# Kernel optimization log

Measured on AMD Instinct MI355X. Metric: run time of the kernel, lower is better.

Reference implementation:

```python
import jax, jax.numpy as jnp
import numpy as np

HID = 768
POS = 768
TGT = 20
LBL = 30522
EPS = 1e-5


def layer_norm(x, g, b):
    mu = jnp.mean(x, axis=-1, keepdims=True)
    var = jnp.mean((x - mu) ** 2, axis=-1, keepdims=True)
    return (x - mu) * jax.lax.rsqrt(var + EPS) * g + b


def setup_inputs() -> dict:
    key = jax.random.key(0)
    ks = jax.random.split(key, 12)
    bs, n_node, num_pairs = 4, 512, 128
    inp = {
        "input_nodes": jax.random.normal(ks[0], (bs, n_node, HID), dtype=jnp.float32),
        "pairs": jax.random.randint(ks[1], (bs, num_pairs, 2), 0, n_node - 1, dtype=jnp.int64),
        "pos_emb": jax.random.normal(ks[2], (TGT, POS), dtype=jnp.float32) * 0.02,
        "W1": jax.random.normal(ks[3], (2 * HID + POS, HID), dtype=jnp.float32) * 0.02,
        "b1": jnp.zeros((HID,), dtype=jnp.float32),
        "g1": jnp.ones((HID,), dtype=jnp.float32),
        "be1": jnp.zeros((HID,), dtype=jnp.float32),
        "W2": jax.random.normal(ks[4], (HID, HID), dtype=jnp.float32) * 0.02,
        "b2": jnp.zeros((HID,), dtype=jnp.float32),
        "g2": jnp.ones((HID,), dtype=jnp.float32),
        "be2": jnp.zeros((HID,), dtype=jnp.float32),
        "Wd": jax.random.normal(ks[5], (HID, LBL), dtype=jnp.float32) * 0.02,
        "bd": jnp.zeros((LBL,), dtype=jnp.float32),
    }
    return inp


def reference(input_nodes, pairs, pos_emb, W1, b1, g1, be1, W2, b2, g2, be2, Wd, bd):
    bs, num_pairs, _ = pairs.shape
    dim = input_nodes.shape[-1]
    left = pairs[:, :, 0] + 1   # [bs, np]
    right = pairs[:, :, 1] + 1
    # gather paired node features: [bs, np, dim]
    lh = jnp.take_along_axis(input_nodes, left[:, :, None], axis=1)
    rh = jnp.take_along_axis(input_nodes, right[:, :, None], axis=1)
    R = bs * num_pairs
    lh = jnp.broadcast_to(lh.reshape(R, 1, dim), (R, TGT, dim))
    rh = jnp.broadcast_to(rh.reshape(R, 1, dim), (R, TGT, dim))
    pe = jnp.broadcast_to(pos_emb[None, :, :], (R, TGT, POS))
    x = jnp.concatenate((lh, rh, pe), axis=-1)  # [R, TGT, 2*HID+POS]
    h = layer_norm(jax.nn.gelu(x @ W1 + b1), g1, be1)
    h = layer_norm(jax.nn.gelu(h @ W2 + b2), g2, be2)
    return h @ Wd + bd  # [R, TGT, LBL]
```

## Files before the change

kernel.cpp:

```cpp
#include <hip/hip_runtime.h>
#include <stdint.h>
#include <math.h>

typedef unsigned short u16;
typedef unsigned int u32;

#define HID   768
#define TGT   20
#define LBL   30522
#define RPAIR 512
#define ROWS  10240
#define KCAT  1536
#define NPAD  30592

typedef float  f32x4  __attribute__((ext_vector_type(4)));
typedef __bf16 bf16x8 __attribute__((ext_vector_type(8)));

__device__ __forceinline__ u16 f2bf(float f) {
  u32 u = __float_as_uint(f);
  u += 0x7fffu + ((u >> 16) & 1u);
  return (u16)(u >> 16);
}
__device__ __forceinline__ float bf2f(u16 h) {
  return __uint_as_float(((u32)h) << 16);
}
__device__ __forceinline__ float gelu_tanh(float x) {
  float x3 = x * x * x;
  float t = tanhf(0.7978845608028654f * (x + 0.044715f * x3));
  return 0.5f * x * (1.0f + t);
}

__device__ __forceinline__ void async16(u16* lds, const u16* g) {
  __builtin_amdgcn_global_load_lds(
      (__attribute__((address_space(1))) void*)const_cast<u16*>(g),
      (__attribute__((address_space(3))) void*)lds,
      16, 0, 0);
}

__global__ __launch_bounds__(256) void tconv_kernel(const float* __restrict__ B,
                                                    u16* __restrict__ Bt,
                                                    int K, int N, int Npad) {
  __shared__ u16 tile[32][34];
  int n0 = blockIdx.x * 32, k0 = blockIdx.y * 32;
  int tx = threadIdx.x & 31, ty = threadIdx.x >> 5;
#pragma unroll
  for (int i = 0; i < 4; i++) {
    int kk = ty + i * 8;
    int k = k0 + kk, n = n0 + tx;
    float v = (k < K && n < N) ? B[(size_t)k * N + n] : 0.0f;
    tile[kk][tx] = f2bf(v);
  }
  __syncthreads();
#pragma unroll
  for (int i = 0; i < 4; i++) {
    int nn = ty + i * 8;
    int n = n0 + nn, k = k0 + tx;
    if (n < Npad && k < K) Bt[(size_t)n * K + k] = tile[tx][nn];
  }
}

__global__ __launch_bounds__(256) void gather_kernel(const float* __restrict__ nodes,
                                                     const int* __restrict__ p32,
                                                     u16* __restrict__ A1) {
  int idx = blockIdx.x * 256 + threadIdx.x;
  if (idx >= RPAIR * KCAT) return;
  bool is64 = ((p32[1] | p32[3] | p32[5] | p32[7] | p32[9] | p32[11] | p32[13] | p32[15]) == 0);
  int r = idx / KCAT, c = idx - r * KCAT;
  int b = r >> 7, p = r & 127;
  int which = (c >= HID) ? 1 : 0;
  int cc = which ? (c - HID) : c;
  int slot = (b * 128 + p) * 2 + which;
  int node = (is64 ? p32[slot * 2] : p32[slot]) + 1;
  float v = nodes[((size_t)(b * 512 + node)) * HID + cc];
  A1[idx] = f2bf(v);
}

__global__ __launch_bounds__(256) void peproj_kernel(const float* __restrict__ pos_emb,
                                                     const float* __restrict__ W1,
                                                     const float* __restrict__ b1,
                                                     float* __restrict__ pep) {
  __shared__ float pe[HID];
  int t = blockIdx.x, tid = threadIdx.x;
  for (int i = tid; i < HID; i += 256) pe[i] = pos_emb[t * HID + i];
  __syncthreads();
  float acc0 = 0.f, acc1 = 0.f, acc2 = 0.f;
  const float* Wp = W1 + (size_t)KCAT * HID;
  for (int k = 0; k < HID; k++) {
    float p = pe[k];
    const float* wr = Wp + (size_t)k * HID;
    acc0 = fmaf(p, wr[tid], acc0);
    acc1 = fmaf(p, wr[tid + 256], acc1);
    acc2 = fmaf(p, wr[tid + 512], acc2);
  }
  pep[t * HID + tid]       = acc0 + b1[tid];
  pep[t * HID + tid + 256] = acc1 + b1[tid + 256];
  pep[t * HID + tid + 512] = acc2 + b1[tid + 512];
}

template <int EPI>
__global__ __launch_bounds__(256) void gemm_bt(const u16* __restrict__ A,
                                               const u16* __restrict__ Bt,
                                               const float* __restrict__ bias,
                                               float* __restrict__ Cf,
                                               u16* __restrict__ Cb,
                                               int N, int K) {
  __shared__ __align__(16) u16 As[128 * 32];
  __shared__ __align__(16) u16 Bs[128 * 32];
  const int tid  = threadIdx.x;
  const int lane = tid & 63;
  const int w    = tid >> 6;
  const int wr   = w >> 1, wc = w & 1;
  const int m0 = blockIdx.y * 128;
  const int n0 = blockIdx.x * 128;

  f32x4 acc[4][4];
  const f32x4 fzero = {0.f, 0.f, 0.f, 0.f};
#pragma unroll
  for (int m = 0; m < 4; m++)
#pragma unroll
    for (int n = 0; n < 4; n++) acc[m][n] = fzero;

  const int srow = lane >> 2;
  const int scol = (lane & 3) * 8;
  const int nkt = K >> 5;

  for (int kt = 0; kt < nkt; ++kt) {
    const int k0 = kt << 5;
#pragma unroll
    for (int j = 0; j < 2; j++) {
      int rbase = w * 32 + j * 16;
      async16(&As[rbase * 32], A + (size_t)(m0 + rbase + srow) * K + k0 + scol);
      async16(&Bs[rbase * 32], Bt + (size_t)(n0 + rbase + srow) * K + k0 + scol);
    }
    asm volatile("s_waitcnt vmcnt(0)" ::: "memory");
    __syncthreads();

    bf16x8 a[4], b[4];
    const int kk = (lane >> 4) * 8;
#pragma unroll
    for (int m = 0; m < 4; m++)
      a[m] = *reinterpret_cast<const bf16x8*>(&As[(wr * 64 + m * 16 + (lane & 15)) * 32 + kk]);
#pragma unroll
    for (int n = 0; n < 4; n++)
      b[n] = *reinterpret_cast<const bf16x8*>(&Bs[(wc * 64 + n * 16 + (lane & 15)) * 32 + kk]);
#pragma unroll
    for (int m = 0; m < 4; m++)
#pragma unroll
      for (int n = 0; n < 4; n++)
        acc[m][n] = __builtin_amdgcn_mfma_f32_16x16x32_bf16(a[m], b[n], acc[m][n], 0, 0, 0);
    __syncthreads();
  }

  const int rr = (lane >> 4) * 4;
  const int cc = lane & 15;
#pragma unroll
  for (int m = 0; m < 4; m++) {
#pragma unroll
    for (int n = 0; n < 4; n++) {
      int col = n0 + wc * 64 + n * 16 + cc;
#pragma unroll
      for (int j = 0; j < 4; j++) {
        int row = m0 + wr * 64 + m * 16 + rr + j;
        float v = acc[m][n][j];
        if (EPI == 0) {
          Cf[(size_t)row * N + col] = v;
        } else if (EPI == 1) {
          v = gelu_tanh(v + bias[col]);
          Cb[(size_t)row * N + col] = f2bf(v);
        } else {
          if (col < N) Cf[(size_t)row * N + col] = v + bias[col];
        }
      }
    }
  }
}

__global__ __launch_bounds__(256) void fuse1_kernel(const float* __restrict__ s,
                                                    const float* __restrict__ pep,
                                                    const float* __restrict__ g1,
                                                    const float* __restrict__ be1,
                                                    u16* __restrict__ h1) {
  __shared__ float red[8];
  int g = blockIdx.x, tid = threadIdx.x;
  int r = g / TGT, t = g - r * TGT;
  const float* sr = s + (size_t)r * HID;
  const float* pt = pep + (size_t)t * HID;
  float y[3], s1 = 0.f, s2 = 0.f;
#pragma unroll
  for (int i = 0; i < 3; i++) {
    int j = tid + i * 256;
    float x = sr[j] + pt[j];
    y[i] = gelu_tanh(x);
    s1 += y[i];
    s2 += y[i] * y[i];
  }
#pragma unroll
  for (int off = 32; off > 0; off >>= 1) {
    s1 += __shfl_down(s1, off);
    s2 += __shfl_down(s2, off);
  }
  if ((tid & 63) == 0) { red[tid >> 6] = s1; red[4 + (tid >> 6)] = s2; }
  __syncthreads();
  float mean = (red[0] + red[1] + red[2] + red[3]) * (1.0f / HID);
  float var  = (red[4] + red[5] + red[6] + red[7]) * (1.0f / HID) - mean * mean;
  float inv  = rsqrtf(var + 1e-5f);
#pragma unroll
  for (int i = 0; i < 3; i++) {
    int j = tid + i * 256;
    h1[(size_t)g * HID + j] = f2bf((y[i] - mean) * inv * g1[j] + be1[j]);
  }
}

__global__ __launch_bounds__(256) void fuse2_kernel(const u16* __restrict__ G,
                                                    const float* __restrict__ g2,
                                                    const float* __restrict__ be2,
                                                    u16* __restrict__ h2) {
  __shared__ float red[8];
  int g = blockIdx.x, tid = threadIdx.x;
  const u16* gr = G + (size_t)g * HID;
  float y[3], s1 = 0.f, s2 = 0.f;
#pragma unroll
  for (int i = 0; i < 3; i++) {
    int j = tid + i * 256;
    y[i] = bf2f(gr[j]);
    s1 += y[i];
    s2 += y[i] * y[i];
  }
#pragma unroll
  for (int off = 32; off > 0; off >>= 1) {
    s1 += __shfl_down(s1, off);
    s2 += __shfl_down(s2, off);
  }
  if ((tid & 63) == 0) { red[tid >> 6] = s1; red[4 + (tid >> 6)] = s2; }
  __syncthreads();
  float mean = (red[0] + red[1] + red[2] + red[3]) * (1.0f / HID);
  float var  = (red[4] + red[5] + red[6] + red[7]) * (1.0f / HID) - mean * mean;
  float inv  = rsqrtf(var + 1e-5f);
#pragma unroll
  for (int i = 0; i < 3; i++) {
    int j = tid + i * 256;
    h2[(size_t)g * HID + j] = f2bf((y[i] - mean) * inv * g2[j] + be2[j]);
  }
}

extern "C" void kernel_launch(void* const* d_in, const int* in_sizes, int n_in,
                              void* d_out, int out_size, void* d_ws, size_t ws_size,
                              hipStream_t stream) {
  const float* input_nodes = (const float*)d_in[0];
  const int*   pairs       = (const int*)d_in[1];
  const float* pos_emb     = (const float*)d_in[2];
  const float* W1  = (const float*)d_in[3];
  const float* b1  = (const float*)d_in[4];
  const float* g1  = (const float*)d_in[5];
  const float* be1 = (const float*)d_in[6];
  const float* W2  = (const float*)d_in[7];
  const float* b2  = (const float*)d_in[8];
  const float* g2  = (const float*)d_in[9];
  const float* be2 = (const float*)d_in[10];
  const float* Wd  = (const float*)d_in[11];
  const float* bd  = (const float*)d_in[12];
  float* out = (float*)d_out;

  char* ws = (char*)d_ws;
  u16*   WdT   = (u16*)(ws + 0);
  u16*   W2T   = (u16*)(ws + 46989312);
  u16*   W1lrT = (u16*)(ws + 48168960);
  u16*   A1    = (u16*)(ws + 50528256);
  float* pep   = (float*)(ws + 52101120);
  float* sbuf  = (float*)(ws + 52162560);
  u16*   h1    = (u16*)(ws + 53735424);
  u16*   G     = (u16*)(ws + 69464064);
  u16*   h2    = (u16*)(ws + 85192704);

  tconv_kernel<<<dim3(956, 24), 256, 0, stream>>>(Wd, WdT, HID, LBL, NPAD);
  tconv_kernel<<<dim3(24, 24), 256, 0, stream>>>(W2, W2T, HID, HID, HID);
  tconv_kernel<<<dim3(24, 48), 256, 0, stream>>>(W1, W1lrT, KCAT, HID, HID);
  gather_kernel<<<dim3((RPAIR * KCAT + 255) / 256), 256, 0, stream>>>(input_nodes, pairs, A1);
  peproj_kernel<<<dim3(TGT), 256, 0, stream>>>(pos_emb, W1, b1, pep);

  gemm_bt<0><<<dim3(6, 4), 256, 0, stream>>>(A1, W1lrT, nullptr, sbuf, nullptr, HID, KCAT);
  fuse1_kernel<<<dim3(ROWS), 256, 0, stream>>>(sbuf, pep, g1, be1, h1);

  gemm_bt<1><<<dim3(6, 80), 256, 0, stream>>>(h1, W2T, b2, nullptr, G, HID, HID);
  fuse2_kernel<<<dim3(ROWS), 256, 0, stream>>>(G, g2, be2, h2);

  gemm_bt<2><<<dim3(239, 80), 256, 0, stream>>>(h2, WdT, bd, out, nullptr, LBL, HID);
}
```

Before: 1.070 ms.

## Replace head GEMM with 256x256-tile double-buffered MFMA kernel

Adds a dedicated 512-thread kernel for the large vocabulary projection. It uses 256x256 output tiles, XOR-swizzled LDS, async global-to-LDS loads, split-phase double buffering with raised MFMA priority, and an XCD-aware block remap. Wd is padded to 30720 columns so tiles divide evenly, and fuse2 now writes its output in place into G, dropping the h2 buffer. The aim is more operand reuse and better overlap of loads with MFMA in the dominant GEMM. The cost is higher register and LDS pressure, and more fragile hand scheduling with explicit waitcnt.

```diff
diff --git a/kernel.cpp b/kernel.cpp
--- a/kernel.cpp
+++ b/kernel.cpp
@@ -11,7 +11,7 @@
 #define RPAIR 512
 #define ROWS  10240
 #define KCAT  1536
-#define NPAD  30592
+#define NPAD2 30720
 
 typedef float  f32x4  __attribute__((ext_vector_type(4)));
 typedef __bf16 bf16x8 __attribute__((ext_vector_type(8)));
@@ -36,6 +36,8 @@
       (__attribute__((address_space(3))) void*)lds,
       16, 0, 0);
 }
+
+#define BARRIER() do { asm volatile("" ::: "memory"); __builtin_amdgcn_s_barrier(); asm volatile("" ::: "memory"); } while (0)
 
 __global__ __launch_bounds__(256) void tconv_kernel(const float* __restrict__ B,
                                                     u16* __restrict__ Bt,
@@ -164,13 +166,159 @@
         float v = acc[m][n][j];
         if (EPI == 0) {
           Cf[(size_t)row * N + col] = v;
-        } else if (EPI == 1) {
+        } else {
           v = gelu_tanh(v + bias[col]);
           Cb[(size_t)row * N + col] = f2bf(v);
-        } else {
-          if (col < N) Cf[(size_t)row * N + col] = v + bias[col];
         }
       }
+    }
+  }
+}
+
+__global__ __launch_bounds__(512, 2) void gemm256_head(const u16* __restrict__ A,
+                                                       const u16* __restrict__ B,
+                                                       const float* __restrict__ bias,
+                                                       float* __restrict__ C) {
+  __shared__ __align__(16) u16 As[2][256 * 64];
+  __shared__ __align__(16) u16 Bs[2][256 * 64];
+  const int tid  = threadIdx.x;
+  const int lane = tid & 63;
+  const int wid  = tid >> 6;
+  const int wm   = wid >> 2;
+  const int wn   = wid & 3;
+
+  int orig = blockIdx.x;
+  int l = (orig & 7) * 600 + (orig >> 3);
+  int mt = l / 120, nt = l - mt * 120;
+  const int m0 = mt * 256, n0 = nt * 256;
+  const int nkt = 12;
+
+  f32x4 acc[8][4];
+  const f32x4 fzero = {0.f, 0.f, 0.f, 0.f};
+#pragma unroll
+  for (int mi = 0; mi < 8; mi++)
+#pragma unroll
+    for (int ni = 0; ni < 4; ni++) acc[mi][ni] = fzero;
+
+  const int sl_r = lane >> 3;
+  const int sl_c = ((lane & 7) ^ sl_r) * 8;
+  auto stage_half = [&](const u16* src, int grow0, u16* ldsReg, int half, int ke0) {
+#pragma unroll
+    for (int j = 0; j < 2; j++) {
+      int rowb = half * 128 + (j * 8 + wid) * 8;
+      const u16* gp = src + (size_t)(grow0 + rowb + sl_r) * 768 + ke0 + sl_c;
+      async16(ldsReg + rowb * 64, gp);
+    }
+  };
+  auto lda = [&](const u16* buf, int mi, int ks) -> bf16x8 {
+    int row = wm * 128 + mi * 16 + (lane & 15);
+    int kch = ks * 4 + (lane >> 4);
+    return *reinterpret_cast<const bf16x8*>(&buf[row * 64 + ((kch ^ (row & 7)) << 3)]);
+  };
+  auto ldb = [&](const u16* buf, int ni, int ks) -> bf16x8 {
+    int row = wn * 64 + ni * 16 + (lane & 15);
+    int kch = ks * 4 + (lane >> 4);
+    return *reinterpret_cast<const bf16x8*>(&buf[row * 64 + ((kch ^ (row & 7)) << 3)]);
+  };
+
+  stage_half(A, m0, As[0], 0, 0);
+  stage_half(A, m0, As[0], 1, 0);
+  stage_half(B, n0, Bs[0], 0, 0);
+  stage_half(B, n0, Bs[0], 1, 0);
+  stage_half(A, m0, As[1], 0, 64);
+  stage_half(A, m0, As[1], 1, 64);
+  asm volatile("s_waitcnt vmcnt(4)" ::: "memory");
+  __builtin_amdgcn_sched_barrier(0);
+  __builtin_amdgcn_s_barrier();
+  asm volatile("" ::: "memory");
+
+  bf16x8 aF[8][2];
+  bf16x8 bF[4][2];
+
+#define MFMA_QUAD(MI0, NI0)                                                        \
+  do {                                                                             \
+    __builtin_amdgcn_s_setprio(1);                                                 \
+    _Pragma("unroll") for (int mi = (MI0); mi < (MI0) + 4; ++mi)                   \
+      _Pragma("unroll") for (int ni = (NI0); ni < (NI0) + 2; ++ni)                 \
+        _Pragma("unroll") for (int ks = 0; ks < 2; ++ks)                           \
+          acc[mi][ni] = __builtin_amdgcn_mfma_f32_16x16x32_bf16(aF[mi][ks], bF[ni][ks], acc[mi][ni], 0, 0, 0); \
+    __builtin_amdgcn_s_setprio(0);                                                 \
+  } while (0)
+
+#define WAIT_LGKM() do { asm volatile("s_waitcnt lgkmcnt(0)" ::: "memory"); __builtin_amdgcn_sched_barrier(0); } while (0)
+
+  for (int t = 0; t < nkt; ++t) {
+    const u16* Ab = As[t & 1];
+    const u16* Bb = Bs[t & 1];
+    u16* Bnext = Bs[(t + 1) & 1];
+    u16* Acur  = As[t & 1];
+    const int ke1 = (t + 1) * 64, ke2 = (t + 2) * 64;
+    const bool sB = (t + 1) < nkt, sA = (t + 2) < nkt;
+
+#pragma unroll
+    for (int mi = 0; mi < 4; ++mi)
+#pragma unroll
+      for (int ks = 0; ks < 2; ++ks) aF[mi][ks] = lda(Ab, mi, ks);
+#pragma unroll
+    for (int ni = 0; ni < 2; ++ni)
+#pragma unroll
+      for (int ks = 0; ks < 2; ++ks) bF[ni][ks] = ldb(Bb, ni, ks);
+    if (sB) stage_half(B, n0, Bnext, 0, ke1);
+    BARRIER();
+    WAIT_LGKM();
+    MFMA_QUAD(0, 0);
+    BARRIER();
+
+#pragma unroll
+    for (int mi = 4; mi < 8; ++mi)
+#pragma unroll
+      for (int ks = 0; ks < 2; ++ks) aF[mi][ks] = lda(Ab, mi, ks);
+    if (sB) stage_half(B, n0, Bnext, 1, ke1);
+    BARRIER();
+    WAIT_LGKM();
+    MFMA_QUAD(4, 0);
+    BARRIER();
+
+#pragma unroll
+    for (int ni = 2; ni < 4; ++ni)
+#pragma unroll
+      for (int ks = 0; ks < 2; ++ks) bF[ni][ks] = ldb(Bb, ni, ks);
+    if (sA) stage_half(A, m0, Acur, 0, ke2);
+    BARRIER();
+    WAIT_LGKM();
+    MFMA_QUAD(4, 2);
+    BARRIER();
+
+    if (sA) stage_half(A, m0, Acur, 1, ke2);
+    BARRIER();
+    MFMA_QUAD(0, 2);
+    if (t + 2 < nkt) {
+      asm volatile("s_waitcnt vmcnt(4)" ::: "memory");
+    } else if (t + 1 < nkt) {
+      asm volatile("s_waitcnt vmcnt(0)" ::: "memory");
+    }
+    __builtin_amdgcn_sched_barrier(0);
+    BARRIER();
+  }
+#undef MFMA_QUAD
+#undef WAIT_LGKM
+
+  const int r0 = m0 + wm * 128;
+  const int c0 = n0 + wn * 64;
+  const int rr = (lane >> 4) * 4;
+  const int ccl = lane & 15;
+#pragma unroll
+  for (int ni = 0; ni < 4; ++ni) {
+    int col = c0 + ni * 16 + ccl;
+    if (col < LBL) {
+      float bv = bias[col];
+#pragma unroll
+      for (int mi = 0; mi < 8; ++mi)
+#pragma unroll
+        for (int j = 0; j < 4; ++j) {
+          int row = r0 + mi * 16 + rr + j;
+          C[(size_t)row * LBL + col] = acc[mi][ni][j] + bv;
+        }
     }
   }
 }
@@ -263,16 +411,15 @@
 
   char* ws = (char*)d_ws;
   u16*   WdT   = (u16*)(ws + 0);
-  u16*   W2T   = (u16*)(ws + 46989312);
-  u16*   W1lrT = (u16*)(ws + 48168960);
-  u16*   A1    = (u16*)(ws + 50528256);
-  float* pep   = (float*)(ws + 52101120);
-  float* sbuf  = (float*)(ws + 52162560);
-  u16*   h1    = (u16*)(ws + 53735424);
-  u16*   G     = (u16*)(ws + 69464064);
-  u16*   h2    = (u16*)(ws + 85192704);
-
-  tconv_kernel<<<dim3(956, 24), 256, 0, stream>>>(Wd, WdT, HID, LBL, NPAD);
+  u16*   W2T   = (u16*)(ws + 47185920);
+  u16*   W1lrT = (u16*)(ws + 48365568);
+  u16*   A1    = (u16*)(ws + 50724864);
+  float* pep   = (float*)(ws + 52297728);
+  float* sbuf  = (float*)(ws + 52359168);
+  u16*   h1    = (u16*)(ws + 53932032);
+  u16*   G     = (u16*)(ws + 69660672);
+
+  tconv_kernel<<<dim3(960, 24), 256, 0, stream>>>(Wd, WdT, HID, LBL, NPAD2);
   tconv_kernel<<<dim3(24, 24), 256, 0, stream>>>(W2, W2T, HID, HID, HID);
   tconv_kernel<<<dim3(24, 48), 256, 0, stream>>>(W1, W1lrT, KCAT, HID, HID);
   gather_kernel<<<dim3((RPAIR * KCAT + 255) / 256), 256, 0, stream>>>(input_nodes, pairs, A1);
@@ -282,7 +429,7 @@
   fuse1_kernel<<<dim3(ROWS), 256, 0, stream>>>(sbuf, pep, g1, be1, h1);
 
   gemm_bt<1><<<dim3(6, 80), 256, 0, stream>>>(h1, W2T, b2, nullptr, G, HID, HID);
-  fuse2_kernel<<<dim3(ROWS), 256, 0, stream>>>(G, g2, be2, h2);
-
-  gemm_bt<2><<<dim3(239, 80), 256, 0, stream>>>(h2, WdT, bd, out, nullptr, LBL, HID);
-}
+  fuse2_kernel<<<dim3(ROWS), 256, 0, stream>>>(G, g2, be2, G);
+
+  gemm256_head<<<dim3(4800), 512, 0, stream>>>(G, WdT, bd, out);
+}
```

Result: slower. 1.296 ms (+21.1%).

## Add dedicated double-buffered head GEMM with XCD-aware tile mapping

Applied to the files above, without the earlier changes.

Replaces the generic gemm_bt<2> used for the large vocabulary projection with a specialized kernel. The new kernel double-buffers LDS with async copies so the next K-tile loads while the current one computes, and hardcodes K=768. It remaps a 1D block id so that each XCD handles a contiguous band of M tiles, which should improve L2 reuse of A. It also hoists the bias load per column and writes fuse2's output in place over G, dropping the separate h2 buffer. In exchange it doubles LDS use per block, which may lower occupancy.

```diff
diff --git a/kernel.cpp b/kernel.cpp
--- a/kernel.cpp
+++ b/kernel.cpp
@@ -164,13 +164,102 @@
         float v = acc[m][n][j];
         if (EPI == 0) {
           Cf[(size_t)row * N + col] = v;
-        } else if (EPI == 1) {
+        } else {
           v = gelu_tanh(v + bias[col]);
           Cb[(size_t)row * N + col] = f2bf(v);
-        } else {
-          if (col < N) Cf[(size_t)row * N + col] = v + bias[col];
         }
       }
+    }
+  }
+}
+
+__global__ __launch_bounds__(256) void gemm128_head(const u16* __restrict__ A,
+                                                    const u16* __restrict__ B,
+                                                    const float* __restrict__ bias,
+                                                    float* __restrict__ C) {
+  __shared__ __align__(16) u16 As[2][128 * 64];
+  __shared__ __align__(16) u16 Bs[2][128 * 64];
+  const int tid  = threadIdx.x;
+  const int lane = tid & 63;
+  const int w    = tid >> 6;
+  const int wr   = w >> 1, wc = w & 1;
+
+  const int bid   = blockIdx.x;
+  const int xcd   = bid & 7;
+  const int idx   = bid >> 3;
+  const int ntile = idx / 10;
+  const int mtile = xcd * 10 + (idx - ntile * 10);
+  const int m0 = mtile * 128;
+  const int n0 = ntile * 128;
+
+  f32x4 acc[4][4];
+  const f32x4 fzero = {0.f, 0.f, 0.f, 0.f};
+#pragma unroll
+  for (int m = 0; m < 4; m++)
+#pragma unroll
+    for (int n = 0; n < 4; n++) acc[m][n] = fzero;
+
+  const int sl_r = lane >> 3;
+  const int sl_c = ((lane & 7) ^ sl_r) * 8;
+  auto stage = [&](int buf, int kt) {
+    const int k0 = kt * 64;
+#pragma unroll
+    for (int j = 0; j < 4; j++) {
+      int rbase = w * 32 + j * 8;
+      async16(&As[buf][rbase * 64], A + (size_t)(m0 + rbase + sl_r) * 768 + k0 + sl_c);
+      async16(&Bs[buf][rbase * 64], B + (size_t)(n0 + rbase + sl_r) * 768 + k0 + sl_c);
+    }
+  };
+  auto lda = [&](const u16* buf, int m, int ks) -> bf16x8 {
+    int row = wr * 64 + m * 16 + (lane & 15);
+    int kch = ks * 4 + (lane >> 4);
+    return *reinterpret_cast<const bf16x8*>(&buf[row * 64 + ((kch ^ (row & 7)) << 3)]);
+  };
+  auto ldb = [&](const u16* buf, int n, int ks) -> bf16x8 {
+    int row = wc * 64 + n * 16 + (lane & 15);
+    int kch = ks * 4 + (lane >> 4);
+    return *reinterpret_cast<const bf16x8*>(&buf[row * 64 + ((kch ^ (row & 7)) << 3)]);
+  };
+
+  const int nkt = 12;
+  stage(0, 0);
+  __syncthreads();
+
+  for (int t = 0; t < nkt; ++t) {
+    const int cur = t & 1;
+    if (t + 1 < nkt) stage(cur ^ 1, t + 1);
+    const u16* Ab = As[cur];
+    const u16* Bb = Bs[cur];
+#pragma unroll
+    for (int ks = 0; ks < 2; ++ks) {
+      bf16x8 a[4], b[4];
+#pragma unroll
+      for (int m = 0; m < 4; m++) a[m] = lda(Ab, m, ks);
+#pragma unroll
+      for (int n = 0; n < 4; n++) b[n] = ldb(Bb, n, ks);
+#pragma unroll
+      for (int m = 0; m < 4; m++)
+#pragma unroll
+        for (int n = 0; n < 4; n++)
+          acc[m][n] = __builtin_amdgcn_mfma_f32_16x16x32_bf16(a[m], b[n], acc[m][n], 0, 0, 0);
+    }
+    __syncthreads();
+  }
+
+  const int rr = (lane >> 4) * 4;
+  const int cc = lane & 15;
+#pragma unroll
+  for (int n = 0; n < 4; n++) {
+    int col = n0 + wc * 64 + n * 16 + cc;
+    if (col < LBL) {
+      float bv = bias[col];
+#pragma unroll
+      for (int m = 0; m < 4; m++)
+#pragma unroll
+        for (int j = 0; j < 4; j++) {
+          int row = m0 + wr * 64 + m * 16 + rr + j;
+          C[(size_t)row * LBL + col] = acc[m][n][j] + bv;
+        }
     }
   }
 }
@@ -270,7 +359,6 @@
   float* sbuf  = (float*)(ws + 52162560);
   u16*   h1    = (u16*)(ws + 53735424);
   u16*   G     = (u16*)(ws + 69464064);
-  u16*   h2    = (u16*)(ws + 85192704);
 
   tconv_kernel<<<dim3(956, 24), 256, 0, stream>>>(Wd, WdT, HID, LBL, NPAD);
   tconv_kernel<<<dim3(24, 24), 256, 0, stream>>>(W2, W2T, HID, HID, HID);
@@ -282,7 +370,7 @@
   fuse1_kernel<<<dim3(ROWS), 256, 0, stream>>>(sbuf, pep, g1, be1, h1);
 
   gemm_bt<1><<<dim3(6, 80), 256, 0, stream>>>(h1, W2T, b2, nullptr, G, HID, HID);
-  fuse2_kernel<<<dim3(ROWS), 256, 0, stream>>>(G, g2, be2, h2);
-
-  gemm_bt<2><<<dim3(239, 80), 256, 0, stream>>>(h2, WdT, bd, out, nullptr, LBL, HID);
-}
+  fuse2_kernel<<<dim3(ROWS), 256, 0, stream>>>(G, g2, be2, G);
+
+  gemm128_head<<<dim3(19120), 256, 0, stream>>>(G, WdT, bd, out);
+}
```

After: 1.287 ms. 20.3% more time.
